# Performance work log

Measured on AMD Instinct MI355X. Metric: run time of the kernel, lower is better.

Reference implementation:

```python
import jax, jax.numpy as jnp
import numpy as np

NX, NY, NZ = 432, 496, 1
D = 64        # num_pt_features
K = 3         # NUM_K
M = 1024      # memory size
BEV = 128     # num_bev_features
NCOORD = 3
NV = 10000    # pillars in scene
NP = 16384    # points in scene
BN_EPS = 1e-3
SHRINK = 0.0025


def hard_shrink_relu(x, lambd, eps=1e-12):
    return jax.nn.relu(x - lambd) * x / (jnp.abs(x - lambd) + eps)


def batchnorm_train(x, gamma, beta, eps=BN_EPS):
    # torch BatchNorm1d training-mode math (biased variance)
    mu = jnp.mean(x, axis=0)
    var = jnp.mean((x - mu) ** 2, axis=0)
    return (x - mu) * jax.lax.rsqrt(var + eps) * gamma + beta


def pdist2(a, b, eps=1e-5):
    # sqrt(eps + |  ||a||^2 + ||b||^2 - 2 a.b |), shape [n1, n2]
    n1 = jnp.sum(a * a, axis=1, keepdims=True)
    n2 = jnp.sum(b * b, axis=1, keepdims=True)
    d2 = n1 + n2.T - 2.0 * (a @ b.T)
    return jnp.sqrt(eps + jnp.abs(d2))


def memory_lookup(x_flat, mem_w, shrink):
    # MemAE-style memory unit: softmax addressing + hard shrink + L1 renorm
    att = jax.nn.softmax(x_flat @ mem_w.T, axis=1)          # [N, M]
    att = hard_shrink_relu(att, shrink)
    att = att / jnp.maximum(jnp.sum(jnp.abs(att), axis=1, keepdims=True), 1e-12)
    return att @ mem_w                                       # [N, D]


def setup_inputs() -> dict:
    key = jax.random.key(0)
    ks = jax.random.split(key, 8)
    rng = np.random.default_rng(0)
    flat = rng.choice(NX * NY, size=NV, replace=False)       # unique BEV cells
    x = (flat % NX).astype(np.int32)
    y = (flat // NX).astype(np.int32)
    coords = jnp.asarray(np.stack([np.zeros(NV, np.int32), x, y,
                                   np.zeros(NV, np.int32)], axis=1))  # (b, x, y, z)
    pc = jax.random.uniform(ks[1], (NP, 4), dtype=jnp.float32)
    point_coords = pc * jnp.array([0.0, NX, NY, 1.0], dtype=jnp.float32)
    return {
        "pillar_features": jax.random.normal(ks[0], (NV, D), dtype=jnp.float32),
        "coords": coords,
        "point_features": jax.random.normal(ks[2], (NP, D), dtype=jnp.float32),
        "point_coords": point_coords,
        "adapt_w": jax.random.normal(ks[3], (BEV // 2, D * K), dtype=jnp.float32) * 0.05,
        "bn1_g": jnp.ones((BEV // 2,), dtype=jnp.float32),
        "bn1_b": jnp.zeros((BEV // 2,), dtype=jnp.float32),
        "weight_w": jax.random.normal(ks[4], (2, BEV // 2), dtype=jnp.float32) * 0.1,
        "bn2_g": jnp.ones((2,), dtype=jnp.float32),
        "bn2_b": jnp.zeros((2,), dtype=jnp.float32),
        "mem_w": jax.random.normal(ks[5], (M, D), dtype=jnp.float32) * 0.1,
    }


def reference(pillar_features, coords, point_features, point_coords,
              adapt_w, bn1_g, bn1_b, weight_w, bn2_g, bn2_b, mem_w):
    nv = pillar_features.shape[0]
    pillars = pillar_features.T                              # [D, nv]

    # --- coord-based retrieval: smallest-K pdist(pillar coords, point coords) ---
    dist = pdist2(coords.astype(jnp.float32), point_coords)  # [nv, np]
    _, idx_c = jax.lax.top_k(-dist, K)                       # [nv, K]
    pillars_positive_coord = point_features[idx_c]           # [nv, K, D]

    # --- feature-based retrieval: top-K of softmax(points @ pillars, axis=0) ---
    score = jax.nn.softmax(point_features @ pillars, axis=0) # [np, nv]
    _, idx_f = jax.lax.top_k(score.T, K)                     # [nv, K]
    points_positive = point_features[idx_f]                  # [nv, K, D]

    # --- memory unit on both branches ---
    out_f = memory_lookup(points_positive.reshape(nv * K, D), mem_w, SHRINK).reshape(nv, K * D)
    out_c = memory_lookup(pillars_positive_coord.reshape(nv * K, D), mem_w, SHRINK).reshape(nv, K * D)

    f = jax.nn.relu(batchnorm_train(out_f @ adapt_w.T, bn1_g, bn1_b))  # [nv, 64]
    c = jax.nn.relu(batchnorm_train(out_c @ adapt_w.T, bn1_g, bn1_b))  # [nv, 64]
    w = jax.nn.softmax(batchnorm_train(pillar_features @ weight_w.T, bn2_g, bn2_b), axis=-1)
    pillars_aug = w[:, :1] * f + w[:, 1:2] * c               # [nv, 64]
    pillars_full = jnp.concatenate([pillars, pillars_aug.T], axis=0)  # [128, nv]

    # --- scatter to BEV canvas ---
    bev_idx = coords[:, 1] + coords[:, 2] * NX + coords[:, 3]
    spatial = jnp.zeros((BEV, NX * NY), dtype=pillar_features.dtype).at[:, bev_idx].set(pillars_full)
    pind = jnp.zeros((NCOORD, NX * NY), dtype=pillar_features.dtype)
    pind = pind.at[0, bev_idx].set(coords[:, 2].astype(jnp.float32))
    pind = pind.at[1, bev_idx].set(coords[:, 3].astype(jnp.float32))
    pind = pind.at[2, bev_idx].set(coords[:, 1].astype(jnp.float32))

    spatial_features = spatial.reshape(1, BEV * NZ, NY, NX)
    spatial_indices = pind.reshape(1, NCOORD * NZ, NY, NX)
    return spatial_features, spatial_indices
```

## Files before the change

kernel.cpp:

```cpp
#include <hip/hip_runtime.h>
#include <math.h>

#define NXc 432
#define NYc 496
#define NVc 10000
#define NPc 16384
#define CELLS (NXc*NYc)
#define SHRINKc 0.0025f
#define NVPAD 10048
#define NBX 27
#define NBY 31
#define NBIN (NBX*NBY)

typedef unsigned short u16;
typedef __attribute__((ext_vector_type(8))) short s16x8;
typedef __attribute__((ext_vector_type(4))) float f32x4;

__device__ __forceinline__ unsigned med3u(unsigned a, unsigned b, unsigned c) {
    unsigned d;
    asm("v_med3_u32 %0, %1, %2, %3" : "=v"(d) : "v"(a), "v"(b), "v"(c));
    return d;
}

__device__ __forceinline__ u16 f2b(float x) {
// ... 18 lines not shown
    if (gid < 260) stats[gid] = 0.f;
    const int N1 = NVPAD * 64;
    const int N2 = N1 + NPc * 64;
    const int N3 = N2 + 65536;
    const int N4 = N3 + 65536;
    if (gid < N1) {
        int v = gid >> 6;
        pillarH[gid] = f2b(v < NVc ? pillar[gid] : 0.f);
    } else if (gid < N2) {
        pfeatH[gid - N1] = f2b(pfeat[gid - N1]);
    } else if (gid < N3) {
        memwH[gid - N2] = f2b(memw[gid - N2]);
    } else if (gid < N4) {
        int i = gid - N3;
        int d = i >> 10, j = i & 1023;
        memwTH[i] = f2b(memw[j * 64 + d]);
    } else {
        int i = gid - N4;
        int c = i >> 6, d = i & 63;
        badaptH[i] = f2b(adapt[(c & 63) * 192 + (c >> 6) * 64 + d]);
    }
}

__global__ __launch_bounds__(1024) void k_binscan(const float* __restrict__ pcoord,
                                                  int* __restrict__ binStart,
                                                  int* __restrict__ binCursor) {
    __shared__ int hcnt[1024];
    __shared__ int sc[1024];
    int t = threadIdx.x;
    hcnt[t] = 0;
    __syncthreads();
    for (int j = t; j < NPc; j += 1024) {
        float qx = pcoord[j * 4 + 1], qy = pcoord[j * 4 + 2];
        int bx = (int)(qx * 0.0625f); if (bx > NBX - 1) bx = NBX - 1;
        int by = (int)(qy * 0.0625f); if (by > NBY - 1) by = NBY - 1;
        atomicAdd(&hcnt[by * NBX + bx], 1);
    }
    __syncthreads();
    int vcount = (t < NBIN) ? hcnt[t] : 0;
    sc[t] = vcount;
    __syncthreads();
    for (int off = 1; off < 1024; off <<= 1) {
        int add = (t >= off) ? sc[t - off] : 0;
        __syncthreads();
        sc[t] += add;
        __syncthreads();
    }
    int excl = sc[t] - vcount;
    if (t <= NBIN) { binStart[t] = excl; binCursor[t] = excl; }
}

__global__ __launch_bounds__(256) void k_binfill(const float* __restrict__ pcoord,
                                                 const int* __restrict__ coords,
                                                 int* __restrict__ binCursor,
                                                 float4* __restrict__ binPC,
                                                 int* __restrict__ cellMap) {
    int j = blockIdx.x * 256 + threadIdx.x;
    float qx = pcoord[j * 4 + 1], qy = pcoord[j * 4 + 2], qz = pcoord[j * 4 + 3];
    int bx = (int)(qx * 0.0625f); if (bx > NBX - 1) bx = NBX - 1;
    int by = (int)(qy * 0.0625f); if (by > NBY - 1) by = NBY - 1;
    int slot = atomicAdd(&binCursor[by * NBX + bx], 1);
    binPC[slot] = make_float4(qx, qy, qz * qz, __uint_as_float((unsigned)j));
    if (j < NVc) {
        int cell = coords[j * 4 + 1] + coords[j * 4 + 2] * NXc + coords[j * 4 + 3];
        cellMap[cell] = j;
    }
}

__global__ __launch_bounds__(64) void k_dist6(const int* __restrict__ coords,
                                              const float4* __restrict__ binPC,
                                              const int* __restrict__ binStart,
                                              int* __restrict__ dIdx6) {
    int v = blockIdx.x * 64 + threadIdx.x;
    if (v >= NVc) return;
    int xi = coords[v * 4 + 1], yi = coords[v * 4 + 2];
    float x = (float)xi, y = (float)yi;
    int bx = xi >> 4; if (bx > NBX - 1) bx = NBX - 1;
    int by = yi >> 4; if (by > NBY - 1) by = NBY - 1;
    unsigned kk[6] = {~0u, ~0u, ~0u, ~0u, ~0u, ~0u};
    for (int r = 0; r < 32; ++r) {
        int x0 = bx - r, x1 = bx + r, y0 = by - r, y1 = by + r;
        for (int cy = y0; cy <= y1; ++cy) {
            if (cy < 0 || cy > NBY - 1) continue;
            int step = (cy == y0 || cy == y1) ? 1 : (x1 > x0 ? x1 - x0 : 1);
            for (int cx = x0; cx <= x1; cx += step) {
                if (cx < 0 || cx > NBX - 1) continue;
                int b = cy * NBX + cx;
                int s0 = binStart[b], s1 = binStart[b + 1];
                for (int s = s0; s < s1; ++s) {
                    float4 p = binPC[s];
                    float e1 = x - p.x, e2 = y - p.y;
                    float d2 = fmaf(e1, e1, fmaf(e2, e2, p.z));
                    unsigned t = (__float_as_uint(d2) & 0xFFFFC000u) | __float_as_uint(p.w);
                    kk[5] = med3u(kk[4], kk[5], t);
                    kk[4] = med3u(kk[3], kk[4], t);
                    kk[3] = med3u(kk[2], kk[3], t);
                    kk[2] = med3u(kk[1], kk[2], t);
                    kk[1] = med3u(kk[0], kk[1], t);
                    kk[0] = kk[0] < t ? kk[0] : t;
                }
            }
        }
        if (kk[2] != ~0u) {
            float d3 = __uint_as_float(kk[2] & 0xFFFFC000u);
            if (256.f * (float)(r * r) > d3 * 1.004f + 1e-3f) break;
        }
    }
#pragma unroll
    for (int j2 = 0; j2 < 6; ++j2) dIdx6[v * 6 + j2] = (int)(kk[j2] & 16383u);
}

__global__ __launch_bounds__(256) void k_score5(const u16* __restrict__ pillarH,
                                                const u16* __restrict__ pfeatH,
                                                int* __restrict__ sIdx) {
    __shared__ u16 BF[2][8192];
    int t = threadIdx.x;
    int w = t >> 6, l = t & 63;
    int lm = l & 15, qd = l >> 4;
    int pb = blockIdx.x * 64;
    int cb = blockIdx.y * 1024;

    const u16* arow = pillarH + (size_t)(pb + 16 * w + lm) * 64 + qd * 8;
    s16x8 a0 = *(const s16x8*)arow;
    s16x8 a1 = *(const s16x8*)(arow + 32);

    int so[4], doff[4];
#pragma unroll
    for (int r = 0; r < 4; ++r) {
        int q = t + 256 * r;
        int row = q >> 3, g = q & 7;
        so[r] = row * 64 + g * 8;
        doff[r] = (((row >> 4) * 8 + g) * 16 + ((row & 15) ^ g)) * 8;
    }
    uint4 pre[4];
    const u16* src = pfeatH + (size_t)cb * 64;
#pragma unroll
    for (int r = 0; r < 4; ++r) pre[r] = *(const uint4*)(src + so[r]);
#pragma unroll
    for (int r = 0; r < 4; ++r) *(uint4*)&BF[0][doff[r]] = pre[r];

    unsigned sk[4][4];
#pragma unroll
    for (int r = 0; r < 4; ++r)
#pragma unroll
        for (int j = 0; j < 4; ++j) sk[r][j] = 0u;

    for (int s = 0; s < 8; ++s) {
        __syncthreads();
        if (s < 7) {
            const u16* s2 = src + (size_t)(s + 1) * 128 * 64;
#pragma unroll
            for (int r = 0; r < 4; ++r) pre[r] = *(const uint4*)(s2 + so[r]);
        }
        const u16* B = &BF[s & 1][0];
#pragma unroll
        for (int pt = 0; pt < 8; ++pt) {
            s16x8 b0 = *(const s16x8*)&B[(((pt * 8 + qd) * 16) + (lm ^ qd)) * 8];
            s16x8 b1 = *(const s16x8*)&B[(((pt * 8 + qd + 4) * 16) + (lm ^ (qd + 4))) * 8];
            f32x4 acc = {256.f, 256.f, 256.f, 256.f};
            acc = __builtin_amdgcn_mfma_f32_16x16x32_bf16(a0, b0, acc, 0, 0, 0);
            acc = __builtin_amdgcn_mfma_f32_16x16x32_bf16(a1, b1, acc, 0, 0, 0);
            unsigned idf = (unsigned)(1023 - (s * 128 + pt * 16 + lm));
#pragma unroll
            for (int r = 0; r < 4; ++r) {
                unsigned key = (__float_as_uint(acc[r]) & 0xFFFFFC00u) | idf;
                sk[r][3] = med3u(sk[r][2], sk[r][3], key);
                sk[r][2] = med3u(sk[r][1], sk[r][2], key);
                sk[r][1] = med3u(sk[r][0], sk[r][1], key);
                sk[r][0] = sk[r][0] > key ? sk[r][0] : key;
            }
        }
        if (s < 7) {
#pragma unroll
            for (int r = 0; r < 4; ++r) *(uint4*)&BF[(s + 1) & 1][doff[r]] = pre[r];
        }
    }
    __syncthreads();
    unsigned* mrg = (unsigned*)&BF[0][0];
#pragma unroll
    for (int r = 0; r < 4; ++r) {
        int row = 16 * w + qd * 4 + r;
        *(uint4*)&mrg[(row * 16 + lm) * 4] = make_uint4(sk[r][0], sk[r][1], sk[r][2], sk[r][3]);
    }
    __syncthreads();
    if (t < 64) {
        int gpr = pb + t;
        unsigned m0 = 0u, m1 = 0u, m2 = 0u, m3 = 0u;
#pragma unroll 4
        for (int cc = 0; cc < 16; ++cc) {
            uint4 v = *(const uint4*)&mrg[(t * 16 + cc) * 4];
#pragma unroll
            for (int j = 0; j < 4; ++j) {
                unsigned x = j == 0 ? v.x : (j == 1 ? v.y : (j == 2 ? v.z : v.w));
                m3 = med3u(m2, m3, x);
                m2 = med3u(m1, m2, x);
                m1 = med3u(m0, m1, x);
                m0 = m0 > x ? m0 : x;
            }
        }
        if (gpr < NVc) {
            int base = (blockIdx.y * NVc + gpr) * 4;
            sIdx[base + 0] = cb + 1023 - (int)(m0 & 1023u);
            sIdx[base + 1] = cb + 1023 - (int)(m1 & 1023u);
            sIdx[base + 2] = cb + 1023 - (int)(m2 & 1023u);
            sIdx[base + 3] = cb + 1023 - (int)(m3 & 1023u);
        }
    }
}

__global__ __launch_bounds__(256) void k_rerank(const float* __restrict__ pillar,
                                                const int* __restrict__ coords,
                                                const float* __restrict__ pfeat,
                                                const float* __restrict__ pcoord,
                                                const int* __restrict__ sIdx,
                                                const int* __restrict__ dIdx6,
                                                int* __restrict__ idx_f,
                                                int* __restrict__ idx_c) {
    int t = threadIdx.x;
    int wv = t >> 6, l = t & 63;
    int v = blockIdx.x * 4 + wv;
    int chunk = l >> 2, slot = l & 3;
    int ps = sIdx[(chunk * NVc + v) * 4 + slot];
    int pd = dIdx6[v * 6 + (l < 6 ? l : 0)];
    double s = 0.0;
#pragma unroll
    for (int i = 0; i < 16; ++i) {
        float4 a = *(const float4*)(pillar + v * 64 + 4 * i);
        float4 b = *(const float4*)(pfeat + ps * 64 + 4 * i);
// ... 10 lines not shown
    for (int k = 0; k < 3; ++k) {
        double bv = sv; int bi = sx;
#pragma unroll
        for (int off = 32; off >= 1; off >>= 1) {
            double ov = __shfl_xor(bv, off);
            int    oi = __shfl_xor(bi, off);
            if (ov > bv || (ov == bv && oi < bi)) { bv = ov; bi = oi; }
        }
        if (l == 0) idx_f[v * 3 + k] = bi;
        if (sx == bi) { sv = -INFINITY; sx = 0x7fffffff; }
    }
    double dv = d2; int dx2 = pd;
    for (int k = 0; k < 3; ++k) {
        double bv = dv; int bi = dx2;
#pragma unroll
        for (int off = 32; off >= 1; off >>= 1) {
            double ov = __shfl_xor(bv, off);
            int    oi = __shfl_xor(bi, off);
            if (ov < bv || (ov == bv && oi < bi)) { bv = ov; bi = oi; }
        }
        if (l == 0) idx_c[v * 3 + k] = bi;
        if (dx2 == bi) { dv = INFINITY; dx2 = 0x7fffffff; }
    }
}

__global__ __launch_bounds__(256) void k_mem2(const u16* __restrict__ pfeatH,
                                              const u16* __restrict__ memwH,
                                              const u16* __restrict__ memwTH,
                                              u16* __restrict__ PoutH) {
    __shared__ u16 WH[8192];
    __shared__ u16 WT[8192];
    __shared__ u16 ST[4][2048];
    int t = threadIdx.x;
    int w = t >> 6, l = t & 63;
    int lm = l & 15, qd = l >> 4;
    int pb = blockIdx.x * 64;

    const u16* arow = pfeatH + (size_t)(pb + 16 * w + lm) * 64 + qd * 8;
    s16x8 a0 = *(const s16x8*)arow;
    s16x8 a1 = *(const s16x8*)(arow + 32);

    float mM[4] = {-INFINITY, -INFINITY, -INFINITY, -INFINITY};
    float Zs[4] = {0.f, 0.f, 0.f, 0.f};

    for (int tile = 0; tile < 8; ++tile) {
        __syncthreads();
#pragma unroll
        for (int r = 0; r < 4; ++r) {
            int q = t + 256 * r;
            int row = q >> 3, g = q & 7;
            uint4 v = *(const uint4*)(memwH + (size_t)(tile * 128 + row) * 64 + g * 8);
            *(uint4*)&WH[(((row >> 4) * 8 + g) * 16 + ((row & 15) ^ g)) * 8] = v;
        }
        __syncthreads();
        f32x4 acc[8];
#pragma unroll
        for (int st = 0; st < 8; ++st) {
            s16x8 b0 = *(const s16x8*)&WH[((st * 8 + qd) * 16 + (lm ^ qd)) * 8];
            s16x8 b1 = *(const s16x8*)&WH[((st * 8 + qd + 4) * 16 + (lm ^ (qd + 4))) * 8];
            f32x4 z = {0.f, 0.f, 0.f, 0.f};
            z = __builtin_amdgcn_mfma_f32_16x16x32_bf16(a0, b0, z, 0, 0, 0);
            z = __builtin_amdgcn_mfma_f32_16x16x32_bf16(a1, b1, z, 0, 0, 0);
            acc[st] = z;
        }
#pragma unroll
        for (int r = 0; r < 4; ++r) {
            float tmax = acc[0][r];
#pragma unroll
            for (int st = 1; st < 8; ++st) tmax = fmaxf(tmax, acc[st][r]);
            float mn = fmaxf(mM[r], tmax);
            float zacc = Zs[r] * __expf(mM[r] - mn);
#pragma unroll
            for (int st = 0; st < 8; ++st) zacc += __expf(acc[st][r] - mn);
            mM[r] = mn; Zs[r] = zacc;
        }
    }
#pragma unroll
    for (int r = 0; r < 4; ++r) {
#pragma unroll
        for (int off = 1; off < 16; off <<= 1) {
            float om = __shfl_xor(mM[r], off);
            float oz = __shfl_xor(Zs[r], off);
            float mn = fmaxf(mM[r], om);
            Zs[r] = Zs[r] * __expf(mM[r] - mn) + oz * __expf(om - mn);
            mM[r] = mn;
        }
    }
    float invZ[4], L1[4] = {0.f, 0.f, 0.f, 0.f};
#pragma unroll
    for (int r = 0; r < 4; ++r) invZ[r] = 1.f / Zs[r];

    f32x4 oacc[4];
#pragma unroll
    for (int n = 0; n < 4; ++n) oacc[n] = (f32x4){0.f, 0.f, 0.f, 0.f};

    for (int tile = 0; tile < 8; ++tile) {
        __syncthreads();
#pragma unroll
        for (int r = 0; r < 4; ++r) {
            int q = t + 256 * r;
            int row = q >> 3, g = q & 7;
            uint4 v = *(const uint4*)(memwH + (size_t)(tile * 128 + row) * 64 + g * 8);
            *(uint4*)&WH[(((row >> 4) * 8 + g) * 16 + ((row & 15) ^ g)) * 8] = v;
        }
#pragma unroll
        for (int r = 0; r < 4; ++r) {
            int q = t + 256 * r;
            int row = q >> 4, g = q & 15;
            uint4 v = *(const uint4*)(memwTH + (size_t)row * 1024 + tile * 128 + g * 8);
            *(uint4*)&WT[(g * 64 + (row ^ g)) * 8] = v;
        }
        __syncthreads();
#pragma unroll
        for (int st = 0; st < 8; ++st) {
            s16x8 b0 = *(const s16x8*)&WH[((st * 8 + qd) * 16 + (lm ^ qd)) * 8];
            s16x8 b1 = *(const s16x8*)&WH[((st * 8 + qd + 4) * 16 + (lm ^ (qd + 4))) * 8];
            f32x4 z = {0.f, 0.f, 0.f, 0.f};
            z = __builtin_amdgcn_mfma_f32_16x16x32_bf16(a0, b0, z, 0, 0, 0);
            z = __builtin_amdgcn_mfma_f32_16x16x32_bf16(a1, b1, z, 0, 0, 0);
            int g2 = st * 2 + (lm >> 3);
#pragma unroll
            for (int r = 0; r < 4; ++r) {
                float e = __expf(z[r] - mM[r]);
                float a = e * invZ[r];
                float tt = a - SHRINKc;
                float sres = fmaxf(tt, 0.f) * a / (fabsf(tt) + 1e-12f);
                L1[r] += sres;
                int rr = qd * 4 + r;
                ST[w][(g2 * 16 + (rr ^ g2)) * 8 + (lm & 7)] = f2b(sres);
            }
        }
#pragma unroll
        for (int ks = 0; ks < 4; ++ks) {
            int g = ks * 4 + qd;
            s16x8 af = *(const s16x8*)&ST[w][(g * 16 + (lm ^ g)) * 8];
#pragma unroll
            for (int n = 0; n < 4; ++n) {
                s16x8 bf = *(const s16x8*)&WT[(g * 64 + ((n * 16 + lm) ^ g)) * 8];
                oacc[n] = __builtin_amdgcn_mfma_f32_16x16x32_bf16(af, bf, oacc[n], 0, 0, 0);
            }
        }
    }
#pragma unroll
    for (int r = 0; r < 4; ++r) {
#pragma unroll
        for (int off = 1; off < 16; off <<= 1) L1[r] += __shfl_xor(L1[r], off);
        L1[r] = 1.f / fmaxf(L1[r], 1e-12f);
    }
#pragma unroll
    for (int n = 0; n < 4; ++n)
#pragma unroll
        for (int r = 0; r < 4; ++r)
            PoutH[(size_t)(pb + 16 * w + qd * 4 + r) * 64 + n * 16 + lm] =
                f2b(oacc[n][r] * L1[r]);
}

__global__ __launch_bounds__(256) void k_proj2(const u16* __restrict__ PoutH,
                                               const u16* __restrict__ badaptH,
                                               float* __restrict__ Q) {
    __shared__ u16 AD[12288];
    int t = threadIdx.x;
    int w = t >> 6, l = t & 63;
    int lm = l & 15, qd = l >> 4;
    int pb = blockIdx.x * 64;
#pragma unroll
    for (int r = 0; r < 6; ++r) {
        int q = t + 256 * r;
        int row = q >> 3, g = q & 7;
        uint4 v = *(const uint4*)(badaptH + (size_t)row * 64 + g * 8);
        *(uint4*)&AD[(((row >> 4) * 8 + g) * 16 + ((row & 15) ^ g)) * 8] = v;
    }
    const u16* arow = PoutH + (size_t)(pb + 16 * w + lm) * 64 + qd * 8;
    s16x8 a0 = *(const s16x8*)arow;
    s16x8 a1 = *(const s16x8*)(arow + 32);
    __syncthreads();
    f32x4 acc[12];
#pragma unroll
// ... 42 lines not shown
        for (int off = 32; off >= 1; off >>= 1) {
            a0 += __shfl_xor(a0, off);
            a1 += __shfl_xor(a1, off);
        }
        if (l == 0) { w_pre[v * 2] = a0; w_pre[v * 2 + 1] = a1; }
        ws0 += a0; wq0 += a0 * a0; ws1 += a1; wq1 += a1 * a1;
    }
    red[0][wv][l] = fs; red[1][wv][l] = fq; red[2][wv][l] = cs; red[3][wv][l] = cq;
    if (l == 0) { redw[wv][0] = ws0; redw[wv][1] = wq0; redw[wv][2] = ws1; redw[wv][3] = wq1; }
    __syncthreads();
    if (wv == 0) {
#pragma unroll
        for (int q = 0; q < 4; ++q) {
            float sum = red[q][0][l] + red[q][1][l] + red[q][2][l] + red[q][3][l];
            atomicAdd(&stats[q * 64 + l], sum);
        }
        if (l < 4) {
            float sum = redw[0][l] + redw[1][l] + redw[2][l] + redw[3][l];
            atomicAdd(&stats[256 + l], sum);
        }
    }
}

__global__ __launch_bounds__(256) void k_aug(const float* __restrict__ f_pre,
                                             const float* __restrict__ c_pre,
                                             const float* __restrict__ w_pre,
                                             const float* __restrict__ stats,
                                             const float* __restrict__ g1,
                                             const float* __restrict__ b1,
                                             const float* __restrict__ g2,
                                             const float* __restrict__ b2,
                                             float* __restrict__ aug) {
    int t = threadIdx.x;
    int wv = t >> 6, l = t & 63;
    int v = blockIdx.x * 4 + wv;
    const float invn = 1.0f / (float)NVc;
    float mf = stats[l] * invn;
    float vf = stats[64 + l] * invn - mf * mf;
    float rf = rsqrtf(vf + 1e-3f);
    float mc = stats[128 + l] * invn;
    float vc = stats[192 + l] * invn - mc * mc;
    float rc = rsqrtf(vc + 1e-3f);
    float mw0 = stats[256] * invn, vw0 = stats[257] * invn - mw0 * mw0;
    float mw1 = stats[258] * invn, vw1 = stats[259] * invn - mw1 * mw1;
    float rw0 = rsqrtf(vw0 + 1e-3f), rw1 = rsqrtf(vw1 + 1e-3f);
    float fb = (f_pre[v * 64 + l] - mf) * rf * g1[l] + b1[l];
    float f = fmaxf(fb, 0.f);
    float cb_ = (c_pre[v * 64 + l] - mc) * rc * g1[l] + b1[l];
    float c = fmaxf(cb_, 0.f);
    float z0 = (w_pre[v * 2] - mw0) * rw0 * g2[0] + b2[0];
    float z1 = (w_pre[v * 2 + 1] - mw1) * rw1 * g2[1] + b2[1];
    float mz = fmaxf(z0, z1);
    float e0 = __expf(z0 - mz), e1 = __expf(z1 - mz);
    float wd = 1.f / (e0 + e1);
    aug[v * 64 + l] = (e0 * wd) * f + (e1 * wd) * c;
}

__global__ __launch_bounds__(256) void k_out(const int* __restrict__ cellMap,
                                             const float* __restrict__ pillar,
                                             const float* __restrict__ aug,
                                             float* __restrict__ out) {
    int c4 = (blockIdx.x * 256 + threadIdx.x) * 4;
    if (c4 >= CELLS) return;
    int4 cm = *(const int4*)(cellMap + c4);
    int f0 = blockIdx.y * 33;
    int f1 = f0 + 33; if (f1 > 131) f1 = 131;
    for (int f = f0; f < f1; ++f) {
        float4 val;
        if (f < 64) {
            val.x = cm.x >= 0 ? pillar[cm.x * 64 + f] : 0.f;
            val.y = cm.y >= 0 ? pillar[cm.y * 64 + f] : 0.f;
            val.z = cm.z >= 0 ? pillar[cm.z * 64 + f] : 0.f;
            val.w = cm.w >= 0 ? pillar[cm.w * 64 + f] : 0.f;
        } else if (f < 128) {
            int fa = f - 64;
            val.x = cm.x >= 0 ? aug[cm.x * 64 + fa] : 0.f;
            val.y = cm.y >= 0 ? aug[cm.y * 64 + fa] : 0.f;
            val.z = cm.z >= 0 ? aug[cm.z * 64 + fa] : 0.f;
            val.w = cm.w >= 0 ? aug[cm.w * 64 + fa] : 0.f;
        } else if (f == 128) {
            val.x = cm.x >= 0 ? (float)((c4 + 0) / NXc) : 0.f;
            val.y = cm.y >= 0 ? (float)((c4 + 1) / NXc) : 0.f;
            val.z = cm.z >= 0 ? (float)((c4 + 2) / NXc) : 0.f;
            val.w = cm.w >= 0 ? (float)((c4 + 3) / NXc) : 0.f;
        } else if (f == 129) {
            val = make_float4(0.f, 0.f, 0.f, 0.f);
        } else {
            val.x = cm.x >= 0 ? (float)((c4 + 0) % NXc) : 0.f;
            val.y = cm.y >= 0 ? (float)((c4 + 1) % NXc) : 0.f;
            val.z = cm.z >= 0 ? (float)((c4 + 2) % NXc) : 0.f;
            val.w = cm.w >= 0 ? (float)((c4 + 3) % NXc) : 0.f;
        }
        *(float4*)(out + (size_t)f * CELLS + c4) = val;
    }
}

extern "C" void kernel_launch(void* const* d_in, const int* in_sizes, int n_in,
                              void* d_out, int out_size, void* d_ws, size_t ws_size,
                              hipStream_t stream) {
    const float* pillar = (const float*)d_in[0];
    const int*   coords = (const int*)d_in[1];
    const float* pfeat  = (const float*)d_in[2];
    const float* pcoord = (const float*)d_in[3];
    const float* adapt  = (const float*)d_in[4];
    const float* bn1g   = (const float*)d_in[5];
    const float* bn1b   = (const float*)d_in[6];
    const float* ww     = (const float*)d_in[7];
    const float* bn2g   = (const float*)d_in[8];
    const float* bn2b   = (const float*)d_in[9];
    const float* memw   = (const float*)d_in[10];
    float* out = (float*)d_out;
    float* ws  = (float*)d_ws;
    u16*   PoutH = (u16*)(ws + 0);
    float* Q     = ws + 1048576;
    int*   sIdx  = (int*)(ws + 4194304);
    int*   binStart  = (int*)(ws + 4834304);
    int*   binCursor = (int*)(ws + 4835200);
    int*   dIdx6     = (int*)(ws + 4836824);
    float4* binPC    = (float4*)(ws + 4896824);
    u16*   memwH   = (u16*)(ws + 4970000);
    u16*   memwTH  = (u16*)(ws + 5002768);
    u16*   badaptH = (u16*)(ws + 5035536);
    int*   idxf  = (int*)(ws + 5474304);
    int*   idxc  = (int*)(ws + 5504304);
    float* fpre  = ws + 5534304;
    float* cpre  = ws + 6174304;
    float* wpre  = ws + 6814304;
    float* stats = ws + 6834304;
    int*   cellMap = (int*)(ws + 6840000);
    float* aug   = ws + 7060000;
    u16* pillarH = (u16*)(ws + 5534304);
    u16* pfeatH  = pillarH + (size_t)NVPAD * 64;

    k_init   <<<7168, 256, 0, stream>>>(pillar, pfeat, memw, adapt, stats, cellMap,
                                        pillarH, pfeatH, memwH, memwTH, badaptH);
    k_binscan<<<1, 1024, 0, stream>>>(pcoord, binStart, binCursor);
    k_binfill<<<64, 256, 0, stream>>>(pcoord, coords, binCursor, binPC, cellMap);
    k_score5 <<<dim3(157, 16), 256, 0, stream>>>(pillarH, pfeatH, sIdx);
    k_dist6  <<<157, 64, 0, stream>>>(coords, binPC, binStart, dIdx6);
    k_rerank <<<2500, 256, 0, stream>>>(pillar, coords, pfeat, pcoord, sIdx, dIdx6, idxf, idxc);
    k_mem2   <<<256, 256, 0, stream>>>(pfeatH, memwH, memwTH, PoutH);
    k_proj2  <<<256, 256, 0, stream>>>(PoutH, badaptH, Q);
    k_gather <<<250, 256, 0, stream>>>(Q, idxf, idxc, pillar, ww, fpre, cpre, wpre, stats);
    k_aug    <<<2500, 256, 0, stream>>>(fpre, cpre, wpre, stats, bn1g, bn1b, bn2g, bn2b, aug);
    k_out    <<<dim3(210, 4), 256, 0, stream>>>(cellMap, pillar, aug, out);
}
```

Measured before the change: 359.5 us.

## Merge independent stages into one heterogeneous launch and fold BN/aug into output

Binning histogram, scan and fill become a single one-block kernel that uses a shared-memory cursor. The memory-lookup, kNN-distance and feature-score stages are packed into one launch, with each block choosing its role from its block index, so the three can run concurrently on the GPU instead of one after another. The batchnorm/softmax augmentation is computed inside the scatter-output kernel, which removes the aug buffer and one launch. The memory-lookup path is rewritten to use a two-pass online softmax over 64-row tiles. The cost is that the BN math is recomputed per output cell and the mixed block roles may hurt occupancy.

```diff
diff --git a/kernel.cpp b/kernel.cpp
--- a/kernel.cpp
+++ b/kernel.cpp
@@ -64,11 +64,14 @@
     }
 }
 
-__global__ __launch_bounds__(1024) void k_binscan(const float* __restrict__ pcoord,
-                                                  int* __restrict__ binStart,
-                                                  int* __restrict__ binCursor) {
+__global__ __launch_bounds__(1024) void k_pre(const float* __restrict__ pcoord,
+                                              const int* __restrict__ coords,
+                                              int* __restrict__ binStart,
+                                              float4* __restrict__ binPC,
+                                              int* __restrict__ cellMap) {
     __shared__ int hcnt[1024];
     __shared__ int sc[1024];
+    __shared__ int cur[1024];
     int t = threadIdx.x;
     hcnt[t] = 0;
     __syncthreads();
@@ -89,163 +92,284 @@
         __syncthreads();
     }
     int excl = sc[t] - vcount;
-    if (t <= NBIN) { binStart[t] = excl; binCursor[t] = excl; }
-}
-
-__global__ __launch_bounds__(256) void k_binfill(const float* __restrict__ pcoord,
-                                                 const int* __restrict__ coords,
-                                                 int* __restrict__ binCursor,
-                                                 float4* __restrict__ binPC,
-                                                 int* __restrict__ cellMap) {
-    int j = blockIdx.x * 256 + threadIdx.x;
-    float qx = pcoord[j * 4 + 1], qy = pcoord[j * 4 + 2], qz = pcoord[j * 4 + 3];
-    int bx = (int)(qx * 0.0625f); if (bx > NBX - 1) bx = NBX - 1;
-    int by = (int)(qy * 0.0625f); if (by > NBY - 1) by = NBY - 1;
-    int slot = atomicAdd(&binCursor[by * NBX + bx], 1);
-    binPC[slot] = make_float4(qx, qy, qz * qz, __uint_as_float((unsigned)j));
-    if (j < NVc) {
+    cur[t] = excl;
+    if (t <= NBIN) binStart[t] = excl;
+    __syncthreads();
+    for (int j = t; j < NPc; j += 1024) {
+        float qx = pcoord[j * 4 + 1], qy = pcoord[j * 4 + 2], qz = pcoord[j * 4 + 3];
+        int bx = (int)(qx * 0.0625f); if (bx > NBX - 1) bx = NBX - 1;
+        int by = (int)(qy * 0.0625f); if (by > NBY - 1) by = NBY - 1;
+        int slot = atomicAdd(&cur[by * NBX + bx], 1);
+        binPC[slot] = make_float4(qx, qy, qz * qz, __uint_as_float((unsigned)j));
+    }
+    for (int j = t; j < NVc; j += 1024) {
         int cell = coords[j * 4 + 1] + coords[j * 4 + 2] * NXc + coords[j * 4 + 3];
         cellMap[cell] = j;
     }
 }
 
-__global__ __launch_bounds__(64) void k_dist6(const int* __restrict__ coords,
-                                              const float4* __restrict__ binPC,
-                                              const int* __restrict__ binStart,
-                                              int* __restrict__ dIdx6) {
-    int v = blockIdx.x * 64 + threadIdx.x;
-    if (v >= NVc) return;
-    int xi = coords[v * 4 + 1], yi = coords[v * 4 + 2];
-    float x = (float)xi, y = (float)yi;
-    int bx = xi >> 4; if (bx > NBX - 1) bx = NBX - 1;
-    int by = yi >> 4; if (by > NBY - 1) by = NBY - 1;
-    unsigned kk[6] = {~0u, ~0u, ~0u, ~0u, ~0u, ~0u};
-    for (int r = 0; r < 32; ++r) {
-        int x0 = bx - r, x1 = bx + r, y0 = by - r, y1 = by + r;
-        for (int cy = y0; cy <= y1; ++cy) {
-            if (cy < 0 || cy > NBY - 1) continue;
-            int step = (cy == y0 || cy == y1) ? 1 : (x1 > x0 ? x1 - x0 : 1);
-            for (int cx = x0; cx <= x1; cx += step) {
-                if (cx < 0 || cx > NBX - 1) continue;
-                int b = cy * NBX + cx;
-                int s0 = binStart[b], s1 = binStart[b + 1];
-                for (int s = s0; s < s1; ++s) {
-                    float4 p = binPC[s];
-                    float e1 = x - p.x, e2 = y - p.y;
-                    float d2 = fmaf(e1, e1, fmaf(e2, e2, p.z));
-                    unsigned t = (__float_as_uint(d2) & 0xFFFFC000u) | __float_as_uint(p.w);
-                    kk[5] = med3u(kk[4], kk[5], t);
-                    kk[4] = med3u(kk[3], kk[4], t);
-                    kk[3] = med3u(kk[2], kk[3], t);
-                    kk[2] = med3u(kk[1], kk[2], t);
-                    kk[1] = med3u(kk[0], kk[1], t);
-                    kk[0] = kk[0] < t ? kk[0] : t;
-                }
-            }
-        }
-        if (kk[2] != ~0u) {
-            float d3 = __uint_as_float(kk[2] & 0xFFFFC000u);
-            if (256.f * (float)(r * r) > d3 * 1.004f + 1e-3f) break;
-        }
-    }
-#pragma unroll
-    for (int j2 = 0; j2 < 6; ++j2) dIdx6[v * 6 + j2] = (int)(kk[j2] & 16383u);
-}
-
-__global__ __launch_bounds__(256) void k_score5(const u16* __restrict__ pillarH,
-                                                const u16* __restrict__ pfeatH,
-                                                int* __restrict__ sIdx) {
-    __shared__ u16 BF[2][8192];
+__global__ __launch_bounds__(256) void k_fused(const u16* __restrict__ pillarH,
+                                               const u16* __restrict__ pfeatH,
+                                               const u16* __restrict__ memwH,
+                                               const u16* __restrict__ memwTH,
+                                               const int* __restrict__ coords,
+                                               const float4* __restrict__ binPC,
+                                               const int* __restrict__ binStart,
+                                               u16* __restrict__ PoutH,
+                                               int* __restrict__ dIdx6,
+                                               int* __restrict__ sIdx) {
+    __shared__ union {
+        u16 bf[2][8192];
+        struct { u16 wh[4096]; u16 wt[4096]; u16 st[4][1024]; } m;
+    } smem;
+    int bid = blockIdx.x;
     int t = threadIdx.x;
     int w = t >> 6, l = t & 63;
     int lm = l & 15, qd = l >> 4;
-    int pb = blockIdx.x * 64;
-    int cb = blockIdx.y * 1024;
-
-    const u16* arow = pillarH + (size_t)(pb + 16 * w + lm) * 64 + qd * 8;
-    s16x8 a0 = *(const s16x8*)arow;
-    s16x8 a1 = *(const s16x8*)(arow + 32);
-
-    int so[4], doff[4];
-#pragma unroll
-    for (int r = 0; r < 4; ++r) {
-        int q = t + 256 * r;
-        int row = q >> 3, g = q & 7;
-        so[r] = row * 64 + g * 8;
-        doff[r] = (((row >> 4) * 8 + g) * 16 + ((row & 15) ^ g)) * 8;
-    }
-    uint4 pre[4];
-    const u16* src = pfeatH + (size_t)cb * 64;
-#pragma unroll
-    for (int r = 0; r < 4; ++r) pre[r] = *(const uint4*)(src + so[r]);
-#pragma unroll
-    for (int r = 0; r < 4; ++r) *(uint4*)&BF[0][doff[r]] = pre[r];
-
-    unsigned sk[4][4];
-#pragma unroll
-    for (int r = 0; r < 4; ++r)
-#pragma unroll
-        for (int j = 0; j < 4; ++j) sk[r][j] = 0u;
-
-    for (int s = 0; s < 8; ++s) {
+
+    if (bid < 256) {
+        int pb = bid * 64;
+        u16* WH = smem.m.wh;
+        u16* WT = smem.m.wt;
+        u16* ST = &smem.m.st[w][0];
+        const u16* arow = pfeatH + (size_t)(pb + 16 * w + lm) * 64 + qd * 8;
+        s16x8 a0 = *(const s16x8*)arow;
+        s16x8 a1 = *(const s16x8*)(arow + 32);
+        float mM[4] = {-INFINITY, -INFINITY, -INFINITY, -INFINITY};
+        float Zs[4] = {0.f, 0.f, 0.f, 0.f};
+        for (int tile = 0; tile < 16; ++tile) {
+            __syncthreads();
+#pragma unroll
+            for (int r = 0; r < 2; ++r) {
+                int q = t + 256 * r;
+                int row = q >> 3, g = q & 7;
+                uint4 v = *(const uint4*)(memwH + (size_t)(tile * 64 + row) * 64 + g * 8);
+                *(uint4*)&WH[(((row >> 4) * 8 + g) * 16 + ((row & 15) ^ g)) * 8] = v;
+            }
+            __syncthreads();
+            f32x4 acc[4];
+#pragma unroll
+            for (int st = 0; st < 4; ++st) {
+                s16x8 b0 = *(const s16x8*)&WH[((st * 8 + qd) * 16 + (lm ^ qd)) * 8];
+                s16x8 b1 = *(const s16x8*)&WH[((st * 8 + qd + 4) * 16 + (lm ^ (qd + 4))) * 8];
+                f32x4 z = {0.f, 0.f, 0.f, 0.f};
+                z = __builtin_amdgcn_mfma_f32_16x16x32_bf16(a0, b0, z, 0, 0, 0);
+                z = __builtin_amdgcn_mfma_f32_16x16x32_bf16(a1, b1, z, 0, 0, 0);
+                acc[st] = z;
+            }
+#pragma unroll
+            for (int r = 0; r < 4; ++r) {
+                float tmax = acc[0][r];
+#pragma unroll
+                for (int st = 1; st < 4; ++st) tmax = fmaxf(tmax, acc[st][r]);
+                float mn = fmaxf(mM[r], tmax);
+                float zacc = Zs[r] * __expf(mM[r] - mn);
+#pragma unroll
+                for (int st = 0; st < 4; ++st) zacc += __expf(acc[st][r] - mn);
+                mM[r] = mn; Zs[r] = zacc;
+            }
+        }
+#pragma unroll
+        for (int r = 0; r < 4; ++r) {
+#pragma unroll
+            for (int off = 1; off < 16; off <<= 1) {
+                float om = __shfl_xor(mM[r], off);
+                float oz = __shfl_xor(Zs[r], off);
+                float mn = fmaxf(mM[r], om);
+                Zs[r] = Zs[r] * __expf(mM[r] - mn) + oz * __expf(om - mn);
+                mM[r] = mn;
+            }
+        }
+        float invZ[4], L1[4] = {0.f, 0.f, 0.f, 0.f};
+#pragma unroll
+        for (int r = 0; r < 4; ++r) invZ[r] = 1.f / Zs[r];
+        f32x4 oacc[4];
+#pragma unroll
+        for (int n = 0; n < 4; ++n) oacc[n] = (f32x4){0.f, 0.f, 0.f, 0.f};
+        for (int tile = 0; tile < 16; ++tile) {
+            __syncthreads();
+#pragma unroll
+            for (int r = 0; r < 2; ++r) {
+                int q = t + 256 * r;
+                int row = q >> 3, g = q & 7;
+                uint4 v = *(const uint4*)(memwH + (size_t)(tile * 64 + row) * 64 + g * 8);
+                *(uint4*)&WH[(((row >> 4) * 8 + g) * 16 + ((row & 15) ^ g)) * 8] = v;
+            }
+#pragma unroll
+            for (int r = 0; r < 2; ++r) {
+                int q = t + 256 * r;
+                int row = q >> 3, g = q & 7;
+                uint4 v = *(const uint4*)(memwTH + (size_t)row * 1024 + tile * 64 + g * 8);
+                *(uint4*)&WT[(g * 64 + (row ^ g)) * 8] = v;
+            }
+            __syncthreads();
+#pragma unroll
+            for (int st = 0; st < 4; ++st) {
+                s16x8 b0 = *(const s16x8*)&WH[((st * 8 + qd) * 16 + (lm ^ qd)) * 8];
+                s16x8 b1 = *(const s16x8*)&WH[((st * 8 + qd + 4) * 16 + (lm ^ (qd + 4))) * 8];
+                f32x4 z = {0.f, 0.f, 0.f, 0.f};
+                z = __builtin_amdgcn_mfma_f32_16x16x32_bf16(a0, b0, z, 0, 0, 0);
+                z = __builtin_amdgcn_mfma_f32_16x16x32_bf16(a1, b1, z, 0, 0, 0);
+                int g2 = st * 2 + (lm >> 3);
+#pragma unroll
+                for (int r = 0; r < 4; ++r) {
+                    float e = __expf(z[r] - mM[r]);
+                    float a = e * invZ[r];
+                    float tt = a - SHRINKc;
+                    float sres = fmaxf(tt, 0.f) * a / (fabsf(tt) + 1e-12f);
+                    L1[r] += sres;
+                    int rr = qd * 4 + r;
+                    ST[(g2 * 16 + (rr ^ g2)) * 8 + (lm & 7)] = f2b(sres);
+                }
+            }
+#pragma unroll
+            for (int ks = 0; ks < 2; ++ks) {
+                int g = ks * 4 + qd;
+                s16x8 af = *(const s16x8*)&ST[(g * 16 + (lm ^ g)) * 8];
+#pragma unroll
+                for (int n = 0; n < 4; ++n) {
+                    s16x8 bf = *(const s16x8*)&WT[(g * 64 + ((n * 16 + lm) ^ g)) * 8];
+                    oacc[n] = __builtin_amdgcn_mfma_f32_16x16x32_bf16(af, bf, oacc[n], 0, 0, 0);
+                }
+            }
+        }
+#pragma unroll
+        for (int r = 0; r < 4; ++r) {
+#pragma unroll
+            for (int off = 1; off < 16; off <<= 1) L1[r] += __shfl_xor(L1[r], off);
+            L1[r] = 1.f / fmaxf(L1[r], 1e-12f);
+        }
+#pragma unroll
+        for (int n = 0; n < 4; ++n)
+#pragma unroll
+            for (int r = 0; r < 4; ++r)
+                PoutH[(size_t)(pb + 16 * w + qd * 4 + r) * 64 + n * 16 + lm] =
+                    f2b(oacc[n][r] * L1[r]);
+    } else if (bid < 296) {
+        int v = (bid - 256) * 256 + t;
+        if (v >= NVc) return;
+        int xi = coords[v * 4 + 1], yi = coords[v * 4 + 2];
+        float x = (float)xi, y = (float)yi;
+        int bx = xi >> 4; if (bx > NBX - 1) bx = NBX - 1;
+        int by = yi >> 4; if (by > NBY - 1) by = NBY - 1;
+        unsigned kk[6] = {~0u, ~0u, ~0u, ~0u, ~0u, ~0u};
+        for (int r = 0; r < 32; ++r) {
+            int x0 = bx - r, x1 = bx + r, y0 = by - r, y1 = by + r;
+            for (int cy = y0; cy <= y1; ++cy) {
+                if (cy < 0 || cy > NBY - 1) continue;
+                int step = (cy == y0 || cy == y1) ? 1 : (x1 > x0 ? x1 - x0 : 1);
+                for (int cx = x0; cx <= x1; cx += step) {
+                    if (cx < 0 || cx > NBX - 1) continue;
+                    int b = cy * NBX + cx;
+                    int s0 = binStart[b], s1 = binStart[b + 1];
+                    for (int s = s0; s < s1; ++s) {
+                        float4 p = binPC[s];
+                        float e1 = x - p.x, e2 = y - p.y;
+                        float d2 = fmaf(e1, e1, fmaf(e2, e2, p.z));
+                        unsigned tk = (__float_as_uint(d2) & 0xFFFFC000u) | __float_as_uint(p.w);
+                        kk[5] = med3u(kk[4], kk[5], tk);
+                        kk[4] = med3u(kk[3], kk[4], tk);
+                        kk[3] = med3u(kk[2], kk[3], tk);
+                        kk[2] = med3u(kk[1], kk[2], tk);
+                        kk[1] = med3u(kk[0], kk[1], tk);
+                        kk[0] = kk[0] < tk ? kk[0] : tk;
+                    }
+                }
+            }
+            if (kk[2] != ~0u) {
+                float d3 = __uint_as_float(kk[2] & 0xFFFFC000u);
+                if (256.f * (float)(r * r) > d3 * 1.004f + 1e-3f) break;
+            }
+        }
+#pragma unroll
+        for (int j2 = 0; j2 < 6; ++j2) dIdx6[v * 6 + j2] = (int)(kk[j2] & 16383u);
+    } else {
+        int sb = bid - 296;
+        int pb = (sb >> 4) * 64;
+        int cb = (sb & 15) * 1024;
+        const u16* arow = pillarH + (size_t)(pb + 16 * w + lm) * 64 + qd * 8;
+        s16x8 a0 = *(const s16x8*)arow;
+        s16x8 a1 = *(const s16x8*)(arow + 32);
+        int so[4], doff[4];
+#pragma unroll
+        for (int r = 0; r < 4; ++r) {
+            int q = t + 256 * r;
+            int row = q >> 3, g = q & 7;
+            so[r] = row * 64 + g * 8;
+            doff[r] = (((row >> 4) * 8 + g) * 16 + ((row & 15) ^ g)) * 8;
+        }
+        uint4 pre[4];
+        const u16* src = pfeatH + (size_t)cb * 64;
+#pragma unroll
+        for (int r = 0; r < 4; ++r) pre[r] = *(const uint4*)(src + so[r]);
+#pragma unroll
+        for (int r = 0; r < 4; ++r) *(uint4*)&smem.bf[0][doff[r]] = pre[r];
+        unsigned sk[4][4];
+#pragma unroll
+        for (int r = 0; r < 4; ++r)
+#pragma unroll
+            for (int j = 0; j < 4; ++j) sk[r][j] = 0u;
+        for (int s = 0; s < 8; ++s) {
+            __syncthreads();
+            if (s < 7) {
+                const u16* s2 = src + (size_t)(s + 1) * 128 * 64;
+#pragma unroll
+                for (int r = 0; r < 4; ++r) pre[r] = *(const uint4*)(s2 + so[r]);
+            }
+            const u16* B = &smem.bf[s & 1][0];
+#pragma unroll
+            for (int pt = 0; pt < 8; ++pt) {
+                s16x8 b0 = *(const s16x8*)&B[(((pt * 8 + qd) * 16) + (lm ^ qd)) * 8];
+                s16x8 b1 = *(const s16x8*)&B[(((pt * 8 + qd + 4) * 16) + (lm ^ (qd + 4))) * 8];
+                f32x4 acc = {256.f, 256.f, 256.f, 256.f};
+                acc = __builtin_amdgcn_mfma_f32_16x16x32_bf16(a0, b0, acc, 0, 0, 0);
+                acc = __builtin_amdgcn_mfma_f32_16x16x32_bf16(a1, b1, acc, 0, 0, 0);
+                unsigned idf = (unsigned)(1023 - (s * 128 + pt * 16 + lm));
+#pragma unroll
+                for (int r = 0; r < 4; ++r) {
+                    unsigned key = (__float_as_uint(acc[r]) & 0xFFFFFC00u) | idf;
+                    sk[r][3] = med3u(sk[r][2], sk[r][3], key);
+                    sk[r][2] = med3u(sk[r][1], sk[r][2], key);
+                    sk[r][1] = med3u(sk[r][0], sk[r][1], key);
+                    sk[r][0] = sk[r][0] > key ? sk[r][0] : key;
+                }
+            }
+            if (s < 7) {
+#pragma unroll
+                for (int r = 0; r < 4; ++r) *(uint4*)&smem.bf[(s + 1) & 1][doff[r]] = pre[r];
+            }
+        }
         __syncthreads();
-        if (s < 7) {
-            const u16* s2 = src + (size_t)(s + 1) * 128 * 64;
-#pragma unroll
-            for (int r = 0; r < 4; ++r) pre[r] = *(const uint4*)(s2 + so[r]);
-        }
-        const u16* B = &BF[s & 1][0];
-#pragma unroll
-        for (int pt = 0; pt < 8; ++pt) {
-            s16x8 b0 = *(const s16x8*)&B[(((pt * 8 + qd) * 16) + (lm ^ qd)) * 8];
-            s16x8 b1 = *(const s16x8*)&B[(((pt * 8 + qd + 4) * 16) + (lm ^ (qd + 4))) * 8];
-            f32x4 acc = {256.f, 256.f, 256.f, 256.f};
-            acc = __builtin_amdgcn_mfma_f32_16x16x32_bf16(a0, b0, acc, 0, 0, 0);
-            acc = __builtin_amdgcn_mfma_f32_16x16x32_bf16(a1, b1, acc, 0, 0, 0);
-            unsigned idf = (unsigned)(1023 - (s * 128 + pt * 16 + lm));
-#pragma unroll
-            for (int r = 0; r < 4; ++r) {
-                unsigned key = (__float_as_uint(acc[r]) & 0xFFFFFC00u) | idf;
-                sk[r][3] = med3u(sk[r][2], sk[r][3], key);
-                sk[r][2] = med3u(sk[r][1], sk[r][2], key);
-                sk[r][1] = med3u(sk[r][0], sk[r][1], key);
-                sk[r][0] = sk[r][0] > key ? sk[r][0] : key;
-            }
-        }
-        if (s < 7) {
-#pragma unroll
-            for (int r = 0; r < 4; ++r) *(uint4*)&BF[(s + 1) & 1][doff[r]] = pre[r];
-        }
-    }
-    __syncthreads();
-    unsigned* mrg = (unsigned*)&BF[0][0];
-#pragma unroll
-    for (int r = 0; r < 4; ++r) {
-        int row = 16 * w + qd * 4 + r;
-        *(uint4*)&mrg[(row * 16 + lm) * 4] = make_uint4(sk[r][0], sk[r][1], sk[r][2], sk[r][3]);
-    }
-    __syncthreads();
-    if (t < 64) {
-        int gpr = pb + t;
-        unsigned m0 = 0u, m1 = 0u, m2 = 0u, m3 = 0u;
+        unsigned* mrg = (unsigned*)&smem.bf[0][0];
+#pragma unroll
+        for (int r = 0; r < 4; ++r) {
+            int row = 16 * w + qd * 4 + r;
+            *(uint4*)&mrg[(row * 16 + lm) * 4] =
+                make_uint4(sk[r][0], sk[r][1], sk[r][2], sk[r][3]);
+        }
+        __syncthreads();
+        if (t < 64) {
+            int gpr = pb + t;
+            unsigned m0 = 0u, m1 = 0u, m2 = 0u, m3 = 0u;
 #pragma unroll 4
-        for (int cc = 0; cc < 16; ++cc) {
-            uint4 v = *(const uint4*)&mrg[(t * 16 + cc) * 4];
-#pragma unroll
-            for (int j = 0; j < 4; ++j) {
-                unsigned x = j == 0 ? v.x : (j == 1 ? v.y : (j == 2 ? v.z : v.w));
-                m3 = med3u(m2, m3, x);
-                m2 = med3u(m1, m2, x);
-                m1 = med3u(m0, m1, x);
-                m0 = m0 > x ? m0 : x;
-            }
-        }
-        if (gpr < NVc) {
-            int base = (blockIdx.y * NVc + gpr) * 4;
-            sIdx[base + 0] = cb + 1023 - (int)(m0 & 1023u);
-            sIdx[base + 1] = cb + 1023 - (int)(m1 & 1023u);
-            sIdx[base + 2] = cb + 1023 - (int)(m2 & 1023u);
-            sIdx[base + 3] = cb + 1023 - (int)(m3 & 1023u);
+            for (int cc = 0; cc < 16; ++cc) {
+                uint4 v = *(const uint4*)&mrg[(t * 16 + cc) * 4];
+#pragma unroll
+                for (int j = 0; j < 4; ++j) {
+                    unsigned x = j == 0 ? v.x : (j == 1 ? v.y : (j == 2 ? v.z : v.w));
+                    m3 = med3u(m2, m3, x);
+                    m2 = med3u(m1, m2, x);
+                    m1 = med3u(m0, m1, x);
+                    m0 = m0 > x ? m0 : x;
+                }
+            }
+            if (gpr < NVc) {
+                int base = ((sb & 15) * NVc + gpr) * 4;
+                sIdx[base + 0] = cb + 1023 - (int)(m0 & 1023u);
+                sIdx[base + 1] = cb + 1023 - (int)(m1 & 1023u);
+                sIdx[base + 2] = cb + 1023 - (int)(m2 & 1023u);
+                sIdx[base + 3] = cb + 1023 - (int)(m3 & 1023u);
+            }
         }
     }
 }
@@ -302,137 +426,6 @@
         if (l == 0) idx_c[v * 3 + k] = bi;
         if (dx2 == bi) { dv = INFINITY; dx2 = 0x7fffffff; }
     }
-}
-
-__global__ __launch_bounds__(256) void k_mem2(const u16* __restrict__ pfeatH,
-                                              const u16* __restrict__ memwH,
-                                              const u16* __restrict__ memwTH,
-                                              u16* __restrict__ PoutH) {
-    __shared__ u16 WH[8192];
-    __shared__ u16 WT[8192];
-    __shared__ u16 ST[4][2048];
-    int t = threadIdx.x;
-    int w = t >> 6, l = t & 63;
-    int lm = l & 15, qd = l >> 4;
-    int pb = blockIdx.x * 64;
-
-    const u16* arow = pfeatH + (size_t)(pb + 16 * w + lm) * 64 + qd * 8;
-    s16x8 a0 = *(const s16x8*)arow;
-    s16x8 a1 = *(const s16x8*)(arow + 32);
-
-    float mM[4] = {-INFINITY, -INFINITY, -INFINITY, -INFINITY};
-    float Zs[4] = {0.f, 0.f, 0.f, 0.f};
-
-    for (int tile = 0; tile < 8; ++tile) {
-        __syncthreads();
-#pragma unroll
-        for (int r = 0; r < 4; ++r) {
-            int q = t + 256 * r;
-            int row = q >> 3, g = q & 7;
-            uint4 v = *(const uint4*)(memwH + (size_t)(tile * 128 + row) * 64 + g * 8);
-            *(uint4*)&WH[(((row >> 4) * 8 + g) * 16 + ((row & 15) ^ g)) * 8] = v;
-        }
-        __syncthreads();
-        f32x4 acc[8];
-#pragma unroll
-        for (int st = 0; st < 8; ++st) {
-            s16x8 b0 = *(const s16x8*)&WH[((st * 8 + qd) * 16 + (lm ^ qd)) * 8];
-            s16x8 b1 = *(const s16x8*)&WH[((st * 8 + qd + 4) * 16 + (lm ^ (qd + 4))) * 8];
-            f32x4 z = {0.f, 0.f, 0.f, 0.f};
-            z = __builtin_amdgcn_mfma_f32_16x16x32_bf16(a0, b0, z, 0, 0, 0);
-            z = __builtin_amdgcn_mfma_f32_16x16x32_bf16(a1, b1, z, 0, 0, 0);
-            acc[st] = z;
-        }
-#pragma unroll
-        for (int r = 0; r < 4; ++r) {
-            float tmax = acc[0][r];
-#pragma unroll
-            for (int st = 1; st < 8; ++st) tmax = fmaxf(tmax, acc[st][r]);
-            float mn = fmaxf(mM[r], tmax);
-            float zacc = Zs[r] * __expf(mM[r] - mn);
-#pragma unroll
-            for (int st = 0; st < 8; ++st) zacc += __expf(acc[st][r] - mn);
-            mM[r] = mn; Zs[r] = zacc;
-        }
-    }
-#pragma unroll
-    for (int r = 0; r < 4; ++r) {
-#pragma unroll
-        for (int off = 1; off < 16; off <<= 1) {
-            float om = __shfl_xor(mM[r], off);
-            float oz = __shfl_xor(Zs[r], off);
-            float mn = fmaxf(mM[r], om);
-            Zs[r] = Zs[r] * __expf(mM[r] - mn) + oz * __expf(om - mn);
-            mM[r] = mn;
-        }
-    }
-    float invZ[4], L1[4] = {0.f, 0.f, 0.f, 0.f};
-#pragma unroll
-    for (int r = 0; r < 4; ++r) invZ[r] = 1.f / Zs[r];
-
-    f32x4 oacc[4];
-#pragma unroll
-    for (int n = 0; n < 4; ++n) oacc[n] = (f32x4){0.f, 0.f, 0.f, 0.f};
-
-    for (int tile = 0; tile < 8; ++tile) {
-        __syncthreads();
-#pragma unroll
-        for (int r = 0; r < 4; ++r) {
-            int q = t + 256 * r;
-            int row = q >> 3, g = q & 7;
-            uint4 v = *(const uint4*)(memwH + (size_t)(tile * 128 + row) * 64 + g * 8);
-            *(uint4*)&WH[(((row >> 4) * 8 + g) * 16 + ((row & 15) ^ g)) * 8] = v;
-        }
-#pragma unroll
-        for (int r = 0; r < 4; ++r) {
-            int q = t + 256 * r;
-            int row = q >> 4, g = q & 15;
-            uint4 v = *(const uint4*)(memwTH + (size_t)row * 1024 + tile * 128 + g * 8);
-            *(uint4*)&WT[(g * 64 + (row ^ g)) * 8] = v;
-        }
-        __syncthreads();
-#pragma unroll
-        for (int st = 0; st < 8; ++st) {
-            s16x8 b0 = *(const s16x8*)&WH[((st * 8 + qd) * 16 + (lm ^ qd)) * 8];
-            s16x8 b1 = *(const s16x8*)&WH[((st * 8 + qd + 4) * 16 + (lm ^ (qd + 4))) * 8];
-            f32x4 z = {0.f, 0.f, 0.f, 0.f};
-            z = __builtin_amdgcn_mfma_f32_16x16x32_bf16(a0, b0, z, 0, 0, 0);
-            z = __builtin_amdgcn_mfma_f32_16x16x32_bf16(a1, b1, z, 0, 0, 0);
-            int g2 = st * 2 + (lm >> 3);
-#pragma unroll
-            for (int r = 0; r < 4; ++r) {
-                float e = __expf(z[r] - mM[r]);
-                float a = e * invZ[r];
-                float tt = a - SHRINKc;
-                float sres = fmaxf(tt, 0.f) * a / (fabsf(tt) + 1e-12f);
-                L1[r] += sres;
-                int rr = qd * 4 + r;
-                ST[w][(g2 * 16 + (rr ^ g2)) * 8 + (lm & 7)] = f2b(sres);
-            }
-        }
-#pragma unroll
-        for (int ks = 0; ks < 4; ++ks) {
-            int g = ks * 4 + qd;
-            s16x8 af = *(const s16x8*)&ST[w][(g * 16 + (lm ^ g)) * 8];
-#pragma unroll
-            for (int n = 0; n < 4; ++n) {
-                s16x8 bf = *(const s16x8*)&WT[(g * 64 + ((n * 16 + lm) ^ g)) * 8];
-                oacc[n] = __builtin_amdgcn_mfma_f32_16x16x32_bf16(af, bf, oacc[n], 0, 0, 0);
-            }
-        }
-    }
-#pragma unroll
-    for (int r = 0; r < 4; ++r) {
-#pragma unroll
-        for (int off = 1; off < 16; off <<= 1) L1[r] += __shfl_xor(L1[r], off);
-        L1[r] = 1.f / fmaxf(L1[r], 1e-12f);
-    }
-#pragma unroll
-    for (int n = 0; n < 4; ++n)
-#pragma unroll
-        for (int r = 0; r < 4; ++r)
-            PoutH[(size_t)(pb + 16 * w + qd * 4 + r) * 64 + n * 16 + lm] =
-                f2b(oacc[n][r] * L1[r]);
 }
 
 __global__ __launch_bounds__(256) void k_proj2(const u16* __restrict__ PoutH,
@@ -521,47 +514,39 @@
     }
 }
 
-__global__ __launch_bounds__(256) void k_aug(const float* __restrict__ f_pre,
-                                             const float* __restrict__ c_pre,
-                                             const float* __restrict__ w_pre,
-                                             const float* __restrict__ stats,
-                                             const float* __restrict__ g1,
-                                             const float* __restrict__ b1,
-                                             const float* __restrict__ g2,
-                                             const float* __restrict__ b2,
-                                             float* __restrict__ aug) {
-    int t = threadIdx.x;
-    int wv = t >> 6, l = t & 63;
-    int v = blockIdx.x * 4 + wv;
+__global__ __launch_bounds__(256) void k_out2(const int* __restrict__ cellMap,
+                                              const float* __restrict__ pillar,
+                                              const float* __restrict__ f_pre,
+                                              const float* __restrict__ c_pre,
+                                              const float* __restrict__ w_pre,
+                                              const float* __restrict__ stats,
+                                              const float* __restrict__ g1,
+                                              const float* __restrict__ b1,
+                                              const float* __restrict__ g2,
+                                              const float* __restrict__ b2,
+                                              float* __restrict__ out) {
+    int c4 = (blockIdx.x * 256 + threadIdx.x) * 4;
+    if (c4 >= CELLS) return;
+    int4 cm = *(const int4*)(cellMap + c4);
     const float invn = 1.0f / (float)NVc;
-    float mf = stats[l] * invn;
-    float vf = stats[64 + l] * invn - mf * mf;
-    float rf = rsqrtf(vf + 1e-3f);
-    float mc = stats[128 + l] * invn;
-    float vc = stats[192 + l] * invn - mc * mc;
-    float rc = rsqrtf(vc + 1e-3f);
     float mw0 = stats[256] * invn, vw0 = stats[257] * invn - mw0 * mw0;
     float mw1 = stats[258] * invn, vw1 = stats[259] * invn - mw1 * mw1;
     float rw0 = rsqrtf(vw0 + 1e-3f), rw1 = rsqrtf(vw1 + 1e-3f);
-    float fb = (f_pre[v * 64 + l] - mf) * rf * g1[l] + b1[l];
-    float f = fmaxf(fb, 0.f);
-    float cb_ = (c_pre[v * 64 + l] - mc) * rc * g1[l] + b1[l];
-    float c = fmaxf(cb_, 0.f);
-    float z0 = (w_pre[v * 2] - mw0) * rw0 * g2[0] + b2[0];
-    float z1 = (w_pre[v * 2 + 1] - mw1) * rw1 * g2[1] + b2[1];
-    float mz = fmaxf(z0, z1);
-    float e0 = __expf(z0 - mz), e1 = __expf(z1 - mz);
-    float wd = 1.f / (e0 + e1);
-    aug[v * 64 + l] = (e0 * wd) * f + (e1 * wd) * c;
-}
-
-__global__ __launch_bounds__(256) void k_out(const int* __restrict__ cellMap,
-                                             const float* __restrict__ pillar,
-                                             const float* __restrict__ aug,
-                                             float* __restrict__ out) {
-    int c4 = (blockIdx.x * 256 + threadIdx.x) * 4;
-    if (c4 >= CELLS) return;
-    int4 cm = *(const int4*)(cellMap + c4);
+    float g20 = g2[0], b20 = b2[0], g21 = g2[1], b21 = b2[1];
+    float w0c[4], w1c[4];
+    int cms[4] = {cm.x, cm.y, cm.z, cm.w};
+#pragma unroll
+    for (int k = 0; k < 4; ++k) {
+        int c = cms[k];
+        if (c >= 0) {
+            float z0 = (w_pre[c * 2] - mw0) * rw0 * g20 + b20;
+            float z1 = (w_pre[c * 2 + 1] - mw1) * rw1 * g21 + b21;
+            float mz = fmaxf(z0, z1);
+            float e0 = __expf(z0 - mz), e1 = __expf(z1 - mz);
+            float wd = 1.f / (e0 + e1);
+            w0c[k] = e0 * wd; w1c[k] = e1 * wd;
+        } else { w0c[k] = 0.f; w1c[k] = 0.f; }
+    }
     int f0 = blockIdx.y * 33;
     int f1 = f0 + 33; if (f1 > 131) f1 = 131;
     for (int f = f0; f < f1; ++f) {
@@ -573,10 +558,21 @@
             val.w = cm.w >= 0 ? pillar[cm.w * 64 + f] : 0.f;
         } else if (f < 128) {
             int fa = f - 64;
-            val.x = cm.x >= 0 ? aug[cm.x * 64 + fa] : 0.f;
-            val.y = cm.y >= 0 ? aug[cm.y * 64 + fa] : 0.f;
-            val.z = cm.z >= 0 ? aug[cm.z * 64 + fa] : 0.f;
-            val.w = cm.w >= 0 ? aug[cm.w * 64 + fa] : 0.f;
+            float mf = stats[fa] * invn;
+            float rf = rsqrtf(stats[64 + fa] * invn - mf * mf + 1e-3f);
+            float mc = stats[128 + fa] * invn;
+            float rc = rsqrtf(stats[192 + fa] * invn - mc * mc + 1e-3f);
+            float gg = g1[fa], bb = b1[fa];
+            float* vv = (float*)&val;
+#pragma unroll
+            for (int k = 0; k < 4; ++k) {
+                int c = cms[k];
+                if (c >= 0) {
+                    float fv = fmaxf((f_pre[c * 64 + fa] - mf) * rf * gg + bb, 0.f);
+                    float cv = fmaxf((c_pre[c * 64 + fa] - mc) * rc * gg + bb, 0.f);
+                    vv[k] = w0c[k] * fv + w1c[k] * cv;
+                } else vv[k] = 0.f;
+            }
         } else if (f == 128) {
             val.x = cm.x >= 0 ? (float)((c4 + 0) / NXc) : 0.f;
             val.y = cm.y >= 0 ? (float)((c4 + 1) / NXc) : 0.f;
@@ -614,7 +610,6 @@
     float* Q     = ws + 1048576;
     int*   sIdx  = (int*)(ws + 4194304);
     int*   binStart  = (int*)(ws + 4834304);
-    int*   binCursor = (int*)(ws + 4835200);
     int*   dIdx6     = (int*)(ws + 4836824);
     float4* binPC    = (float4*)(ws + 4896824);
     u16*   memwH   = (u16*)(ws + 4970000);
@@ -627,20 +622,17 @@
     float* wpre  = ws + 6814304;
     float* stats = ws + 6834304;
     int*   cellMap = (int*)(ws + 6840000);
-    float* aug   = ws + 7060000;
     u16* pillarH = (u16*)(ws + 5534304);
     u16* pfeatH  = pillarH + (size_t)NVPAD * 64;
 
-    k_init   <<<7168, 256, 0, stream>>>(pillar, pfeat, memw, adapt, stats, cellMap,
-                                        pillarH, pfeatH, memwH, memwTH, badaptH);
-    k_binscan<<<1, 1024, 0, stream>>>(pcoord, binStart, binCursor);
-    k_binfill<<<64, 256, 0, stream>>>(pcoord, coords, binCursor, binPC, cellMap);
-    k_score5 <<<dim3(157, 16), 256, 0, stream>>>(pillarH, pfeatH, sIdx);
-    k_dist6  <<<157, 64, 0, stream>>>(coords, binPC, binStart, dIdx6);
-    k_rerank <<<2500, 256, 0, stream>>>(pillar, coords, pfeat, pcoord, sIdx, dIdx6, idxf, idxc);
-    k_mem2   <<<256, 256, 0, stream>>>(pfeatH, memwH, memwTH, PoutH);
-    k_proj2  <<<256, 256, 0, stream>>>(PoutH, badaptH, Q);
-    k_gather <<<250, 256, 0, stream>>>(Q, idxf, idxc, pillar, ww, fpre, cpre, wpre, stats);
-    k_aug    <<<2500, 256, 0, stream>>>(fpre, cpre, wpre, stats, bn1g, bn1b, bn2g, bn2b, aug);
-    k_out    <<<dim3(210, 4), 256, 0, stream>>>(cellMap, pillar, aug, out);
-}
+    k_init  <<<7168, 256, 0, stream>>>(pillar, pfeat, memw, adapt, stats, cellMap,
+                                       pillarH, pfeatH, memwH, memwTH, badaptH);
+    k_pre   <<<1, 1024, 0, stream>>>(pcoord, coords, binStart, binPC, cellMap);
+    k_fused <<<2808, 256, 0, stream>>>(pillarH, pfeatH, memwH, memwTH, coords,
+                                       binPC, binStart, PoutH, dIdx6, sIdx);
+    k_rerank<<<2500, 256, 0, stream>>>(pillar, coords, pfeat, pcoord, sIdx, dIdx6, idxf, idxc);
+    k_proj2 <<<256, 256, 0, stream>>>(PoutH, badaptH, Q);
+    k_gather<<<250, 256, 0, stream>>>(Q, idxf, idxc, pillar, ww, fpre, cpre, wpre, stats);
+    k_out2  <<<dim3(210, 4), 256, 0, stream>>>(cellMap, pillar, fpre, cpre, wpre, stats,
+                                               bn1g, bn1b, bn2g, bn2b, out);
+}
```

Result: faster. 338.4 us (-5.9%).
